# Optimization experiments

Hardware: AMD Instinct MI355X
Metric: run time of the kernel (lower is better)

## Reference

```python
import jax, jax.numpy as jnp
import numpy as np

TWO_PI = 2.0 * np.pi

def ringify(x):
    # wrap values to [-pi, pi)
    return (x + np.pi) % TWO_PI - np.pi

def complex_mean(x, axes):
    # circular mean direction: atan2(sum sin, sum ringify(cos))
    dir_x = ringify(jnp.cos(x)).sum(axis=axes)
    dir_y = jnp.sin(x).sum(axis=axes)
    return jnp.arctan2(dir_y, dir_x)

def setup_inputs() -> dict:
    key = jax.random.key(0)
    k1, k2, k3, k4 = jax.random.split(key, 4)
    B = 4096
    return {
        "x": jax.random.normal(k1, (B, 1, 28, 28), dtype=jnp.float32),
        "conv1_w": jax.random.normal(k2, (4, 1, 2, 2), dtype=jnp.float32),
        "conv2_w": jax.random.normal(k3, (8, 4, 4, 4), dtype=jnp.float32),
        "ff_w": jax.random.normal(k4, (288, 10), dtype=jnp.float32),
    }

def reference(x, conv1_w, conv2_w, ff_w):
    B = x.shape[0]
    x = ringify(x).reshape(B, 1, 28, 28)

    # --- ring conv1: 2x2 kernel, stride 2 (non-overlapping patches) ---
    # [B,1,28,28] -> [B,14,14,1,2,2]  (matches unfold(2,2,2).unfold(3,2,2).permute)
    p1 = x.reshape(B, 1, 14, 2, 14, 2).transpose(0, 2, 4, 1, 3, 5)
    w1 = conv1_w.transpose(1, 2, 3, 0)            # [1,2,2,4]
    d1 = ringify(p1[..., None] - w1)              # [B,14,14,1,2,2,4]
    h1 = complex_mean(d1, (3, 4, 5))              # [B,14,14,4]

    # --- ring conv2: 4x4 kernel, stride 2 (overlapping patches) ---
    h1 = h1.transpose(0, 3, 1, 2)                 # [B,4,14,14]
    idx = (jnp.arange(6) * 2)[:, None] + jnp.arange(4)[None, :]  # [6,4] window rows/cols
    p2 = h1[:, :, idx, :][:, :, :, :, idx]        # [B,4,6,4,6,4]
    p2 = p2.transpose(0, 2, 4, 1, 3, 5)           # [B,6,6,4,4,4]
    w2 = conv2_w.transpose(1, 2, 3, 0)            # [4,4,4,8]
    d2 = ringify(p2[..., None] - w2)              # [B,6,6,4,4,4,8]
    h2 = complex_mean(d2, (3, 4, 5))              # [B,6,6,8]

    # --- ring feed-forward ---
    f = h2.reshape(B, 288)
    d3 = ringify(f[:, :, None] - ff_w)            # [B,288,10]
    out = complex_mean(d3, (1,))                  # [B,10]
    return jnp.sin(out)
```

## Files before the change

kernel.cpp:

```cpp
#include <hip/hip_runtime.h>
#include <math.h>

#define FFT_OFF 0
#define W2_OFF 2880
#define W1_OFF 3400

__global__ void precompute_trig(const float* __restrict__ w1,
                                const float* __restrict__ w2,
                                const float* __restrict__ ff,
                                float2* __restrict__ ws) {
    int idx = blockIdx.x * blockDim.x + threadIdx.x;
    if (idx < 2880) {
        int k = idx / 10, n = idx % 10;
        float s, c; sincosf(ff[idx], &s, &c);
        ws[FFT_OFF + n * 288 + k] = make_float2(c, s);
    } else if (idx < 3392) {
        int i = idx - 2880;
        int oc = i >> 6, e = i & 63;
        float s, c; sincosf(w2[i], &s, &c);
        ws[W2_OFF + (oc >> 1) * 130 + e * 2 + (oc & 1)] = make_float2(c, s);
    } else if (idx < 3408) {
        int i = idx - 3392;
        float s, c; sincosf(w1[i], &s, &c);
        ws[W1_OFF + i] = make_float2(c, s);
    }
}

__global__ __launch_bounds__(320) void ringnn_kernel(
    const float* __restrict__ x,
    const float2* __restrict__ ws,
    float* __restrict__ out)
{
    __shared__ __align__(16) float2 trig2[520];
    __shared__ __align__(16) float2 sc1[1008];
    __shared__ __align__(16) float2 sc2[288];
    const int tid = threadIdx.x;
    const float2* __restrict__ fft = ws + FFT_OFF;
    const float2* __restrict__ w1t = ws + W1_OFF;

    int pi = (tid % 196) / 14, pj = tid % 14;
    float2 r0 = make_float2(0.f, 0.f), r1 = make_float2(0.f, 0.f);
    if (tid < 196) {
        const float* xb = x + (size_t)blockIdx.x * 784;
        r0 = *(const float2*)(xb + (2 * pi) * 28 + 2 * pj);
        r1 = *(const float2*)(xb + (2 * pi + 1) * 28 + 2 * pj);
    }

    if (tid < 260) ((float4*)trig2)[tid] = ((const float4*)(ws + W2_OFF))[tid];

    if (tid < 196) {
        float sx[4], cx[4];
        __sincosf(r0.x, &sx[0], &cx[0]);
        __sincosf(r0.y, &sx[1], &cx[1]);
        __sincosf(r1.x, &sx[2], &cx[2]);
        __sincosf(r1.y, &sx[3], &cx[3]);
        #pragma unroll
        for (int oc = 0; oc < 4; oc++) {
            float4 wa = *(const float4*)(w1t + oc * 4);
            float4 wb = *(const float4*)(w1t + oc * 4 + 2);
            float Y = 0.f, X = 0.f;
            Y = fmaf(sx[0], wa.x, fmaf(-cx[0], wa.y, Y));
            X = fmaf(cx[0], wa.x, fmaf( sx[0], wa.y, X));
            Y = fmaf(sx[1], wa.z, fmaf(-cx[1], wa.w, Y));
            X = fmaf(cx[1], wa.z, fmaf( sx[1], wa.w, X));
            Y = fmaf(sx[2], wb.x, fmaf(-cx[2], wb.y, Y));
            X = fmaf(cx[2], wb.x, fmaf( sx[2], wb.y, X));
            Y = fmaf(sx[3], wb.z, fmaf(-cx[3], wb.w, Y));
            X = fmaf(cx[3], wb.z, fmaf( sx[3], wb.w, X));
            float inv = rsqrtf(fmaxf(fmaf(X, X, Y * Y), 1e-30f));
            sc1[oc * 252 + pi * 18 + pj] = make_float2(Y * inv, X * inv);
        }
    }
    __syncthreads();

    if (tid < 96) {
        int r = tid;
        int oi = r >> 4, ojg = (r >> 3) & 1, ocp = (r >> 1) & 3, hf = r & 1;
        const float2* wbp = trig2 + ocp * 130;
        float aY[3][2] = {{0.f,0.f},{0.f,0.f},{0.f,0.f}};
        float aX[3][2] = {{0.f,0.f},{0.f,0.f},{0.f,0.f}};
        #pragma unroll
        for (int ch = 0; ch < 4; ch++) {
            #pragma unroll
            for (int kk = 0; kk < 2; kk++) {
                int ki = hf * 2 + kk;
                int base = ch * 252 + (oi * 2 + ki) * 18 + ojg * 6;
                float4 f0 = *(const float4*)(sc1 + base);
                float4 f1 = *(const float4*)(sc1 + base + 2);
                float4 f2 = *(const float4*)(sc1 + base + 4);
                float4 f3 = *(const float4*)(sc1 + base + 6);
                float ss[8] = {f0.x,f0.z,f1.x,f1.z,f2.x,f2.z,f3.x,f3.z};
                float cc[8] = {f0.y,f0.w,f1.y,f1.w,f2.y,f2.w,f3.y,f3.w};
                int e0 = ch * 16 + ki * 4;
                #pragma unroll
                for (int kj = 0; kj < 4; kj++) {
                    float4 wv = *(const float4*)(wbp + (e0 + kj) * 2);
                    #pragma unroll
                    for (int ojl = 0; ojl < 3; ojl++) {
                        float s = ss[ojl * 2 + kj], c = cc[ojl * 2 + kj];
                        aY[ojl][0] = fmaf(s, wv.x, fmaf(-c, wv.y, aY[ojl][0]));
                        aX[ojl][0] = fmaf(c, wv.x, fmaf( s, wv.y, aX[ojl][0]));
                        aY[ojl][1] = fmaf(s, wv.z, fmaf(-c, wv.w, aY[ojl][1]));
                        aX[ojl][1] = fmaf(c, wv.z, fmaf( s, wv.w, aX[ojl][1]));
                    }
                }
            }
        }
        #pragma unroll
        for (int ojl = 0; ojl < 3; ojl++) {
            float y0 = aY[ojl][0]; y0 += __shfl_xor(y0, 1);
            float y1 = aY[ojl][1]; y1 += __shfl_xor(y1, 1);
            float x0 = aX[ojl][0]; x0 += __shfl_xor(x0, 1);
            float x1 = aX[ojl][1]; x1 += __shfl_xor(x1, 1);
            float Y = hf ? y1 : y0;
            float X = hf ? x1 : x0;
            float inv = rsqrtf(fmaxf(fmaf(X, X, Y * Y), 1e-30f));
            int p = oi * 6 + ojg * 3 + ojl;
            sc2[p * 8 + ocp * 2 + hf] = make_float2(Y * inv, X * inv);
        }
    }
    __syncthreads();

    {
        int n = tid >> 5, s = tid & 31;
        const float2* wn = fft + n * 288;
        float Y = 0.f, X = 0.f;
        #pragma unroll
        for (int i = 0; i < 9; i++) {
            int k = i * 32 + s;
            float2 sc = sc2[k];
            float2 w = wn[k];
            Y = fmaf(sc.x, w.x, fmaf(-sc.y, w.y, Y));
            X = fmaf(sc.y, w.x, fmaf( sc.x, w.y, X));
        }
        #pragma unroll
        for (int off = 16; off > 0; off >>= 1) {
            Y += __shfl_down(Y, off, 32);
            X += __shfl_down(X, off, 32);
        }
        if (s == 0) {
            out[(size_t)blockIdx.x * 10 + n] =
                Y * rsqrtf(fmaxf(fmaf(X, X, Y * Y), 1e-30f));
        }
    }
}

extern "C" void kernel_launch(void* const* d_in, const int* in_sizes, int n_in,
                              void* d_out, int out_size, void* d_ws, size_t ws_size,
                              hipStream_t stream) {
    const float* x  = (const float*)d_in[0];
    const float* w1 = (const float*)d_in[1];
    const float* w2 = (const float*)d_in[2];
    const float* ff = (const float*)d_in[3];
    float* out = (float*)d_out;
    const int B = in_sizes[0] / 784;

    float2* ws = (float2*)d_ws;
    precompute_trig<<<14, 256, 0, stream>>>(w1, w2, ff, ws);
    ringnn_kernel<<<B, 320, 0, stream>>>(x, ws, out);
}
```

Measured before the change: 86.49 us.

## Shrink blocks to 128 threads and give each thread multiple work items

The block size drops from 320 to 128 threads. Each thread now handles up to two conv1 positions and up to three feed-forward reduction slots, and the weight staging becomes a strided loop. The intent is to stop wasting idle lanes in the phases that used only part of the 320 threads, and to fit more blocks per CU. In exchange the conv1 and final phases are serialized per thread, while the conv2 phase still uses only 96 threads.

```diff
diff --git a/kernel.cpp b/kernel.cpp
--- a/kernel.cpp
+++ b/kernel.cpp
@@ -26,7 +26,34 @@
     }
 }
 
-__global__ __launch_bounds__(320) void ringnn_kernel(
+__device__ __forceinline__ void conv1_pos(float2 r0, float2 r1,
+                                          const float2* __restrict__ w1t,
+                                          float2* __restrict__ sc1,
+                                          int pi, int pj) {
+    float sx[4], cx[4];
+    __sincosf(r0.x, &sx[0], &cx[0]);
+    __sincosf(r0.y, &sx[1], &cx[1]);
+    __sincosf(r1.x, &sx[2], &cx[2]);
+    __sincosf(r1.y, &sx[3], &cx[3]);
+    #pragma unroll
+    for (int oc = 0; oc < 4; oc++) {
+        float4 wa = *(const float4*)(w1t + oc * 4);
+        float4 wb = *(const float4*)(w1t + oc * 4 + 2);
+        float Y = 0.f, X = 0.f;
+        Y = fmaf(sx[0], wa.x, fmaf(-cx[0], wa.y, Y));
+        X = fmaf(cx[0], wa.x, fmaf( sx[0], wa.y, X));
+        Y = fmaf(sx[1], wa.z, fmaf(-cx[1], wa.w, Y));
+        X = fmaf(cx[1], wa.z, fmaf( sx[1], wa.w, X));
+        Y = fmaf(sx[2], wb.x, fmaf(-cx[2], wb.y, Y));
+        X = fmaf(cx[2], wb.x, fmaf( sx[2], wb.y, X));
+        Y = fmaf(sx[3], wb.z, fmaf(-cx[3], wb.w, Y));
+        X = fmaf(cx[3], wb.z, fmaf( sx[3], wb.w, X));
+        float inv = rsqrtf(fmaxf(fmaf(X, X, Y * Y), 1e-30f));
+        sc1[oc * 252 + pi * 18 + pj] = make_float2(Y * inv, X * inv);
+    }
+}
+
+__global__ __launch_bounds__(128, 4) void ringnn_kernel(
     const float* __restrict__ x,
     const float2* __restrict__ ws,
     float* __restrict__ out)
@@ -38,39 +65,24 @@
     const float2* __restrict__ fft = ws + FFT_OFF;
     const float2* __restrict__ w1t = ws + W1_OFF;
 
-    int pi = (tid % 196) / 14, pj = tid % 14;
-    float2 r0 = make_float2(0.f, 0.f), r1 = make_float2(0.f, 0.f);
-    if (tid < 196) {
-        const float* xb = x + (size_t)blockIdx.x * 784;
-        r0 = *(const float2*)(xb + (2 * pi) * 28 + 2 * pj);
-        r1 = *(const float2*)(xb + (2 * pi + 1) * 28 + 2 * pj);
+    const float* xb = x + (size_t)blockIdx.x * 784;
+    const int pi0 = tid / 14, pj0 = tid % 14;
+    float2 a0 = *(const float2*)(xb + (2 * pi0) * 28 + 2 * pj0);
+    float2 a1 = *(const float2*)(xb + (2 * pi0 + 1) * 28 + 2 * pj0);
+    const int p1 = tid + 128;
+    int pi1 = 0, pj1 = 0;
+    float2 b0 = make_float2(0.f, 0.f), b1 = make_float2(0.f, 0.f);
+    if (p1 < 196) {
+        pi1 = p1 / 14; pj1 = p1 % 14;
+        b0 = *(const float2*)(xb + (2 * pi1) * 28 + 2 * pj1);
+        b1 = *(const float2*)(xb + (2 * pi1 + 1) * 28 + 2 * pj1);
     }
 
-    if (tid < 260) ((float4*)trig2)[tid] = ((const float4*)(ws + W2_OFF))[tid];
+    for (int i = tid; i < 260; i += 128)
+        ((float4*)trig2)[i] = ((const float4*)(ws + W2_OFF))[i];
 
-    if (tid < 196) {
-        float sx[4], cx[4];
-        __sincosf(r0.x, &sx[0], &cx[0]);
-        __sincosf(r0.y, &sx[1], &cx[1]);
-        __sincosf(r1.x, &sx[2], &cx[2]);
-        __sincosf(r1.y, &sx[3], &cx[3]);
-        #pragma unroll
-        for (int oc = 0; oc < 4; oc++) {
-            float4 wa = *(const float4*)(w1t + oc * 4);
-            float4 wb = *(const float4*)(w1t + oc * 4 + 2);
-            float Y = 0.f, X = 0.f;
-            Y = fmaf(sx[0], wa.x, fmaf(-cx[0], wa.y, Y));
-            X = fmaf(cx[0], wa.x, fmaf( sx[0], wa.y, X));
-            Y = fmaf(sx[1], wa.z, fmaf(-cx[1], wa.w, Y));
-            X = fmaf(cx[1], wa.z, fmaf( sx[1], wa.w, X));
-            Y = fmaf(sx[2], wb.x, fmaf(-cx[2], wb.y, Y));
-            X = fmaf(cx[2], wb.x, fmaf( sx[2], wb.y, X));
-            Y = fmaf(sx[3], wb.z, fmaf(-cx[3], wb.w, Y));
-            X = fmaf(cx[3], wb.z, fmaf( sx[3], wb.w, X));
-            float inv = rsqrtf(fmaxf(fmaf(X, X, Y * Y), 1e-30f));
-            sc1[oc * 252 + pi * 18 + pj] = make_float2(Y * inv, X * inv);
-        }
-    }
+    conv1_pos(a0, a1, w1t, sc1, pi0, pj0);
+    if (p1 < 196) conv1_pos(b0, b1, w1t, sc1, pi1, pj1);
     __syncthreads();
 
     if (tid < 96) {
@@ -121,26 +133,30 @@
     }
     __syncthreads();
 
-    {
-        int n = tid >> 5, s = tid & 31;
-        const float2* wn = fft + n * 288;
-        float Y = 0.f, X = 0.f;
-        #pragma unroll
-        for (int i = 0; i < 9; i++) {
-            int k = i * 32 + s;
-            float2 sc = sc2[k];
-            float2 w = wn[k];
-            Y = fmaf(sc.x, w.x, fmaf(-sc.y, w.y, Y));
-            X = fmaf(sc.y, w.x, fmaf( sc.x, w.y, X));
-        }
-        #pragma unroll
-        for (int off = 16; off > 0; off >>= 1) {
-            Y += __shfl_down(Y, off, 32);
-            X += __shfl_down(X, off, 32);
-        }
-        if (s == 0) {
-            out[(size_t)blockIdx.x * 10 + n] =
-                Y * rsqrtf(fmaxf(fmaf(X, X, Y * Y), 1e-30f));
+    #pragma unroll
+    for (int rr = 0; rr < 3; rr++) {
+        int idx = tid + (rr << 7);
+        if (idx < 320) {
+            int n = idx >> 5, s = idx & 31;
+            const float2* wn = fft + n * 288;
+            float Y = 0.f, X = 0.f;
+            #pragma unroll
+            for (int i = 0; i < 9; i++) {
+                int k = i * 32 + s;
+                float2 sc = sc2[k];
+                float2 w = wn[k];
+                Y = fmaf(sc.x, w.x, fmaf(-sc.y, w.y, Y));
+                X = fmaf(sc.y, w.x, fmaf( sc.x, w.y, X));
+            }
+            #pragma unroll
+            for (int off = 16; off > 0; off >>= 1) {
+                Y += __shfl_down(Y, off, 32);
+                X += __shfl_down(X, off, 32);
+            }
+            if (s == 0) {
+                out[(size_t)blockIdx.x * 10 + n] =
+                    Y * rsqrtf(fmaxf(fmaf(X, X, Y * Y), 1e-30f));
+            }
         }
     }
 }
@@ -157,5 +173,5 @@
 
     float2* ws = (float2*)d_ws;
     precompute_trig<<<14, 256, 0, stream>>>(w1, w2, ff, ws);
-    ringnn_kernel<<<B, 320, 0, stream>>>(x, ws, out);
+    ringnn_kernel<<<B, 128, 0, stream>>>(x, ws, out);
 }
```

After: 85.01 us. No clear change (-1.7%).

## Process one image per wavefront, three per block, dropping block barriers

Applied to the files above, without the earlier changes.

Each 64-lane wavefront now handles one whole image, looping over conv1 positions, conv2 tasks and FF outputs, and each block holds three images with per-wave shared scratch. The __syncthreads between stages are replaced by a wave-local lgkmcnt wait, which removes block-wide barriers and the idle lanes left by the 320-thread layout. The cost is more serial work per wave, a larger shared-memory footprint per block, and reliance on the wave executing in lockstep for correct ordering through LDS.

```diff
diff --git a/kernel.cpp b/kernel.cpp
--- a/kernel.cpp
+++ b/kernel.cpp
@@ -26,103 +26,132 @@
     }
 }
 
-__global__ __launch_bounds__(320) void ringnn_kernel(
+__device__ __forceinline__ void conv1_pos(float2 r0, float2 r1,
+                                          const float2* __restrict__ w1t,
+                                          float2* __restrict__ sc1,
+                                          int pi, int pj) {
+    float sx[4], cx[4];
+    __sincosf(r0.x, &sx[0], &cx[0]);
+    __sincosf(r0.y, &sx[1], &cx[1]);
+    __sincosf(r1.x, &sx[2], &cx[2]);
+    __sincosf(r1.y, &sx[3], &cx[3]);
+    #pragma unroll
+    for (int oc = 0; oc < 4; oc++) {
+        float4 wa = *(const float4*)(w1t + oc * 4);
+        float4 wb = *(const float4*)(w1t + oc * 4 + 2);
+        float Y = 0.f, X = 0.f;
+        Y = fmaf(sx[0], wa.x, fmaf(-cx[0], wa.y, Y));
+        X = fmaf(cx[0], wa.x, fmaf( sx[0], wa.y, X));
+        Y = fmaf(sx[1], wa.z, fmaf(-cx[1], wa.w, Y));
+        X = fmaf(cx[1], wa.z, fmaf( sx[1], wa.w, X));
+        Y = fmaf(sx[2], wb.x, fmaf(-cx[2], wb.y, Y));
+        X = fmaf(cx[2], wb.x, fmaf( sx[2], wb.y, X));
+        Y = fmaf(sx[3], wb.z, fmaf(-cx[3], wb.w, Y));
+        X = fmaf(cx[3], wb.z, fmaf( sx[3], wb.w, X));
+        float inv = rsqrtf(fmaxf(fmaf(X, X, Y * Y), 1e-30f));
+        sc1[oc * 252 + pi * 18 + pj] = make_float2(Y * inv, X * inv);
+    }
+}
+
+__global__ __launch_bounds__(192, 4) void ringnn_kernel(
     const float* __restrict__ x,
     const float2* __restrict__ ws,
-    float* __restrict__ out)
+    float* __restrict__ out,
+    int nImg)
 {
     __shared__ __align__(16) float2 trig2[520];
-    __shared__ __align__(16) float2 sc1[1008];
-    __shared__ __align__(16) float2 sc2[288];
+    __shared__ __align__(16) float2 sc1s[3 * 1008];
+    __shared__ __align__(16) float2 sc2s[3 * 288];
     const int tid = threadIdx.x;
+    const int wave = tid >> 6, lane = tid & 63;
+    const int img = blockIdx.x * 3 + wave;
     const float2* __restrict__ fft = ws + FFT_OFF;
     const float2* __restrict__ w1t = ws + W1_OFF;
+    const bool live = (img < nImg);
 
-    int pi = (tid % 196) / 14, pj = tid % 14;
-    float2 r0 = make_float2(0.f, 0.f), r1 = make_float2(0.f, 0.f);
-    if (tid < 196) {
-        const float* xb = x + (size_t)blockIdx.x * 784;
-        r0 = *(const float2*)(xb + (2 * pi) * 28 + 2 * pj);
-        r1 = *(const float2*)(xb + (2 * pi + 1) * 28 + 2 * pj);
+    const float* xp = x + (size_t)img * 784;
+    float2 xa[4], xb[4];
+    #pragma unroll
+    for (int r = 0; r < 4; r++) {
+        int pos = lane + (r << 6);
+        xa[r] = make_float2(0.f, 0.f); xb[r] = make_float2(0.f, 0.f);
+        if (live && pos < 196) {
+            int pi = pos / 14, pj = pos % 14;
+            xa[r] = *(const float2*)(xp + (2 * pi) * 28 + 2 * pj);
+            xb[r] = *(const float2*)(xp + (2 * pi + 1) * 28 + 2 * pj);
+        }
     }
 
-    if (tid < 260) ((float4*)trig2)[tid] = ((const float4*)(ws + W2_OFF))[tid];
+    for (int i = tid; i < 260; i += 192)
+        ((float4*)trig2)[i] = ((const float4*)(ws + W2_OFF))[i];
+    __syncthreads();
+    if (!live) return;
 
-    if (tid < 196) {
-        float sx[4], cx[4];
-        __sincosf(r0.x, &sx[0], &cx[0]);
-        __sincosf(r0.y, &sx[1], &cx[1]);
-        __sincosf(r1.x, &sx[2], &cx[2]);
-        __sincosf(r1.y, &sx[3], &cx[3]);
-        #pragma unroll
-        for (int oc = 0; oc < 4; oc++) {
-            float4 wa = *(const float4*)(w1t + oc * 4);
-            float4 wb = *(const float4*)(w1t + oc * 4 + 2);
-            float Y = 0.f, X = 0.f;
-            Y = fmaf(sx[0], wa.x, fmaf(-cx[0], wa.y, Y));
-            X = fmaf(cx[0], wa.x, fmaf( sx[0], wa.y, X));
-            Y = fmaf(sx[1], wa.z, fmaf(-cx[1], wa.w, Y));
-            X = fmaf(cx[1], wa.z, fmaf( sx[1], wa.w, X));
-            Y = fmaf(sx[2], wb.x, fmaf(-cx[2], wb.y, Y));
-            X = fmaf(cx[2], wb.x, fmaf( sx[2], wb.y, X));
-            Y = fmaf(sx[3], wb.z, fmaf(-cx[3], wb.w, Y));
-            X = fmaf(cx[3], wb.z, fmaf( sx[3], wb.w, X));
-            float inv = rsqrtf(fmaxf(fmaf(X, X, Y * Y), 1e-30f));
-            sc1[oc * 252 + pi * 18 + pj] = make_float2(Y * inv, X * inv);
-        }
+    float2* __restrict__ sc1 = sc1s + wave * 1008;
+    float2* __restrict__ sc2 = sc2s + wave * 288;
+
+    #pragma unroll
+    for (int r = 0; r < 4; r++) {
+        int pos = lane + (r << 6);
+        if (pos < 196) conv1_pos(xa[r], xb[r], w1t, sc1, pos / 14, pos % 14);
     }
-    __syncthreads();
+    asm volatile("s_waitcnt lgkmcnt(0)" ::: "memory");
 
-    if (tid < 96) {
-        int r = tid;
-        int oi = r >> 4, ojg = (r >> 3) & 1, ocp = (r >> 1) & 3, hf = r & 1;
-        const float2* wbp = trig2 + ocp * 130;
-        float aY[3][2] = {{0.f,0.f},{0.f,0.f},{0.f,0.f}};
-        float aX[3][2] = {{0.f,0.f},{0.f,0.f},{0.f,0.f}};
-        #pragma unroll
-        for (int ch = 0; ch < 4; ch++) {
+    #pragma unroll
+    for (int rr = 0; rr < 2; rr++) {
+        int task = lane + (rr << 6);
+        if (task < 96) {
+            int oi = task >> 4, ojg = (task >> 3) & 1, ocp = (task >> 1) & 3, hf = task & 1;
+            const float2* wbp = trig2 + ocp * 130;
+            float aY[3][2] = {{0.f,0.f},{0.f,0.f},{0.f,0.f}};
+            float aX[3][2] = {{0.f,0.f},{0.f,0.f},{0.f,0.f}};
             #pragma unroll
-            for (int kk = 0; kk < 2; kk++) {
-                int ki = hf * 2 + kk;
-                int base = ch * 252 + (oi * 2 + ki) * 18 + ojg * 6;
-                float4 f0 = *(const float4*)(sc1 + base);
-                float4 f1 = *(const float4*)(sc1 + base + 2);
-                float4 f2 = *(const float4*)(sc1 + base + 4);
-                float4 f3 = *(const float4*)(sc1 + base + 6);
-                float ss[8] = {f0.x,f0.z,f1.x,f1.z,f2.x,f2.z,f3.x,f3.z};
-                float cc[8] = {f0.y,f0.w,f1.y,f1.w,f2.y,f2.w,f3.y,f3.w};
-                int e0 = ch * 16 + ki * 4;
+            for (int ch = 0; ch < 4; ch++) {
                 #pragma unroll
-                for (int kj = 0; kj < 4; kj++) {
-                    float4 wv = *(const float4*)(wbp + (e0 + kj) * 2);
+                for (int kk = 0; kk < 2; kk++) {
+                    int ki = hf * 2 + kk;
+                    int base = ch * 252 + (oi * 2 + ki) * 18 + ojg * 6;
+                    float4 f0 = *(const float4*)(sc1 + base);
+                    float4 f1 = *(const float4*)(sc1 + base + 2);
+                    float4 f2 = *(const float4*)(sc1 + base + 4);
+                    float4 f3 = *(const float4*)(sc1 + base + 6);
+                    float ss[8] = {f0.x,f0.z,f1.x,f1.z,f2.x,f2.z,f3.x,f3.z};
+                    float cc[8] = {f0.y,f0.w,f1.y,f1.w,f2.y,f2.w,f3.y,f3.w};
+                    int e0 = ch * 16 + ki * 4;
                     #pragma unroll
-                    for (int ojl = 0; ojl < 3; ojl++) {
-                        float s = ss[ojl * 2 + kj], c = cc[ojl * 2 + kj];
-                        aY[ojl][0] = fmaf(s, wv.x, fmaf(-c, wv.y, aY[ojl][0]));
-                        aX[ojl][0] = fmaf(c, wv.x, fmaf( s, wv.y, aX[ojl][0]));
-                        aY[ojl][1] = fmaf(s, wv.z, fmaf(-c, wv.w, aY[ojl][1]));
-                        aX[ojl][1] = fmaf(c, wv.z, fmaf( s, wv.w, aX[ojl][1]));
+                    for (int kj = 0; kj < 4; kj++) {
+                        float4 wv = *(const float4*)(wbp + (e0 + kj) * 2);
+                        #pragma unroll
+                        for (int ojl = 0; ojl < 3; ojl++) {
+                            float s = ss[ojl * 2 + kj], c = cc[ojl * 2 + kj];
+                            aY[ojl][0] = fmaf(s, wv.x, fmaf(-c, wv.y, aY[ojl][0]));
+                            aX[ojl][0] = fmaf(c, wv.x, fmaf( s, wv.y, aX[ojl][0]));
+                            aY[ojl][1] = fmaf(s, wv.z, fmaf(-c, wv.w, aY[ojl][1]));
+                            aX[ojl][1] = fmaf(c, wv.z, fmaf( s, wv.w, aX[ojl][1]));
+                        }
                     }
                 }
             }
-        }
-        #pragma unroll
-        for (int ojl = 0; ojl < 3; ojl++) {
-            float y0 = aY[ojl][0]; y0 += __shfl_xor(y0, 1);
-            float y1 = aY[ojl][1]; y1 += __shfl_xor(y1, 1);
-            float x0 = aX[ojl][0]; x0 += __shfl_xor(x0, 1);
-            float x1 = aX[ojl][1]; x1 += __shfl_xor(x1, 1);
-            float Y = hf ? y1 : y0;
-            float X = hf ? x1 : x0;
-            float inv = rsqrtf(fmaxf(fmaf(X, X, Y * Y), 1e-30f));
-            int p = oi * 6 + ojg * 3 + ojl;
-            sc2[p * 8 + ocp * 2 + hf] = make_float2(Y * inv, X * inv);
+            #pragma unroll
+            for (int ojl = 0; ojl < 3; ojl++) {
+                float y0 = aY[ojl][0]; y0 += __shfl_xor(y0, 1);
+                float y1 = aY[ojl][1]; y1 += __shfl_xor(y1, 1);
+                float x0 = aX[ojl][0]; x0 += __shfl_xor(x0, 1);
+                float x1 = aX[ojl][1]; x1 += __shfl_xor(x1, 1);
+                float Y = hf ? y1 : y0;
+                float X = hf ? x1 : x0;
+                float inv = rsqrtf(fmaxf(fmaf(X, X, Y * Y), 1e-30f));
+                int p = oi * 6 + ojg * 3 + ojl;
+                sc2[p * 8 + ocp * 2 + hf] = make_float2(Y * inv, X * inv);
+            }
         }
     }
-    __syncthreads();
+    asm volatile("s_waitcnt lgkmcnt(0)" ::: "memory");
 
-    {
-        int n = tid >> 5, s = tid & 31;
+    #pragma unroll
+    for (int rr = 0; rr < 5; rr++) {
+        int task = lane + (rr << 6);
+        int n = task >> 5, s = task & 31;
         const float2* wn = fft + n * 288;
         float Y = 0.f, X = 0.f;
         #pragma unroll
@@ -139,7 +168,7 @@
             X += __shfl_down(X, off, 32);
         }
         if (s == 0) {
-            out[(size_t)blockIdx.x * 10 + n] =
+            out[(size_t)img * 10 + n] =
                 Y * rsqrtf(fmaxf(fmaf(X, X, Y * Y), 1e-30f));
         }
     }
@@ -157,5 +186,5 @@
 
     float2* ws = (float2*)d_ws;
     precompute_trig<<<14, 256, 0, stream>>>(w1, w2, ff, ws);
-    ringnn_kernel<<<B, 320, 0, stream>>>(x, ws, out);
+    ringnn_kernel<<<(B + 2) / 3, 192, 0, stream>>>(x, ws, out, B);
 }
```

New measurement: 86.16 us. No clear change (-0.4%).

## Process eight images per block with warp-per-image stages and DPP reductions

Applied to the files above, without the earlier changes.

Restructures the ring-NN kernel so each 256-thread block handles eight images instead of one. Conv1 runs one 32-lane group per image, conv2 assigns a wave per output-channel pair with weights read from global memory instead of staged in LDS, and the feed-forward stage uses a DPP-based 32-lane reduction per image. The aim is to raise thread utilisation (the old layout left many threads idle per stage) and amortise launch and sync overhead across images. In exchange it uses much more LDS per block and caps occupancy via launch bounds. It also assumes the batch size is divisible by 8.

```diff
diff --git a/kernel.cpp b/kernel.cpp
--- a/kernel.cpp
+++ b/kernel.cpp
@@ -4,6 +4,8 @@
 #define FFT_OFF 0
 #define W2_OFF 2880
 #define W1_OFF 3400
+#define S1 786
+#define S2 292
 
 __global__ void precompute_trig(const float* __restrict__ w1,
                                 const float* __restrict__ w2,
@@ -26,121 +28,152 @@
     }
 }
 
-__global__ __launch_bounds__(320) void ringnn_kernel(
+__device__ __forceinline__ void conv1_pos(float2 r0, float2 r1,
+                                          const float2* __restrict__ w1t,
+                                          float2* __restrict__ sc1,
+                                          int pi, int pj) {
+    float sx[4], cx[4];
+    __sincosf(r0.x, &sx[0], &cx[0]);
+    __sincosf(r0.y, &sx[1], &cx[1]);
+    __sincosf(r1.x, &sx[2], &cx[2]);
+    __sincosf(r1.y, &sx[3], &cx[3]);
+    #pragma unroll
+    for (int oc = 0; oc < 4; oc++) {
+        float4 wa = *(const float4*)(w1t + oc * 4);
+        float4 wb = *(const float4*)(w1t + oc * 4 + 2);
+        float Y = 0.f, X = 0.f;
+        Y = fmaf(sx[0], wa.x, fmaf(-cx[0], wa.y, Y));
+        X = fmaf(cx[0], wa.x, fmaf( sx[0], wa.y, X));
+        Y = fmaf(sx[1], wa.z, fmaf(-cx[1], wa.w, Y));
+        X = fmaf(cx[1], wa.z, fmaf( sx[1], wa.w, X));
+        Y = fmaf(sx[2], wb.x, fmaf(-cx[2], wb.y, Y));
+        X = fmaf(cx[2], wb.x, fmaf( sx[2], wb.y, X));
+        Y = fmaf(sx[3], wb.z, fmaf(-cx[3], wb.w, Y));
+        X = fmaf(cx[3], wb.z, fmaf( sx[3], wb.w, X));
+        float inv = rsqrtf(fmaxf(fmaf(X, X, Y * Y), 1e-30f));
+        sc1[oc * 196 + pi * 14 + pj] = make_float2(Y * inv, X * inv);
+    }
+}
+
+template <int CTRL>
+__device__ __forceinline__ float dpp_add(float v) {
+    return v + __int_as_float(__builtin_amdgcn_mov_dpp(
+                   __float_as_int(v), CTRL, 0xF, 0xF, true));
+}
+__device__ __forceinline__ float reduce32(float v) {
+    v = dpp_add<0x111>(v);
+    v = dpp_add<0x112>(v);
+    v = dpp_add<0x114>(v);
+    v = dpp_add<0x118>(v);
+    v = dpp_add<0x142>(v);
+    return v;
+}
+
+__global__ __launch_bounds__(256, 2) void ringnn_kernel(
     const float* __restrict__ x,
     const float2* __restrict__ ws,
     float* __restrict__ out)
 {
-    __shared__ __align__(16) float2 trig2[520];
-    __shared__ __align__(16) float2 sc1[1008];
-    __shared__ __align__(16) float2 sc2[288];
+    __shared__ __align__(16) float2 sc1[8 * S1];
+    __shared__ __align__(16) float2 sc2[8 * S2];
     const int tid = threadIdx.x;
+    const int g = tid >> 5, s = tid & 31;
+    const size_t imgBase = (size_t)blockIdx.x * 8;
     const float2* __restrict__ fft = ws + FFT_OFF;
     const float2* __restrict__ w1t = ws + W1_OFF;
 
-    int pi = (tid % 196) / 14, pj = tid % 14;
-    float2 r0 = make_float2(0.f, 0.f), r1 = make_float2(0.f, 0.f);
-    if (tid < 196) {
-        const float* xb = x + (size_t)blockIdx.x * 784;
-        r0 = *(const float2*)(xb + (2 * pi) * 28 + 2 * pj);
-        r1 = *(const float2*)(xb + (2 * pi + 1) * 28 + 2 * pj);
-    }
-
-    if (tid < 260) ((float4*)trig2)[tid] = ((const float4*)(ws + W2_OFF))[tid];
-
-    if (tid < 196) {
-        float sx[4], cx[4];
-        __sincosf(r0.x, &sx[0], &cx[0]);
-        __sincosf(r0.y, &sx[1], &cx[1]);
-        __sincosf(r1.x, &sx[2], &cx[2]);
-        __sincosf(r1.y, &sx[3], &cx[3]);
+    {
+        const float* xp = x + (imgBase + g) * 784;
+        float2* s1 = sc1 + g * S1;
         #pragma unroll
-        for (int oc = 0; oc < 4; oc++) {
-            float4 wa = *(const float4*)(w1t + oc * 4);
-            float4 wb = *(const float4*)(w1t + oc * 4 + 2);
-            float Y = 0.f, X = 0.f;
-            Y = fmaf(sx[0], wa.x, fmaf(-cx[0], wa.y, Y));
-            X = fmaf(cx[0], wa.x, fmaf( sx[0], wa.y, X));
-            Y = fmaf(sx[1], wa.z, fmaf(-cx[1], wa.w, Y));
-            X = fmaf(cx[1], wa.z, fmaf( sx[1], wa.w, X));
-            Y = fmaf(sx[2], wb.x, fmaf(-cx[2], wb.y, Y));
-            X = fmaf(cx[2], wb.x, fmaf( sx[2], wb.y, X));
-            Y = fmaf(sx[3], wb.z, fmaf(-cx[3], wb.w, Y));
-            X = fmaf(cx[3], wb.z, fmaf( sx[3], wb.w, X));
-            float inv = rsqrtf(fmaxf(fmaf(X, X, Y * Y), 1e-30f));
-            sc1[oc * 252 + pi * 18 + pj] = make_float2(Y * inv, X * inv);
-        }
-    }
-    __syncthreads();
-
-    if (tid < 96) {
-        int r = tid;
-        int oi = r >> 4, ojg = (r >> 3) & 1, ocp = (r >> 1) & 3, hf = r & 1;
-        const float2* wbp = trig2 + ocp * 130;
-        float aY[3][2] = {{0.f,0.f},{0.f,0.f},{0.f,0.f}};
-        float aX[3][2] = {{0.f,0.f},{0.f,0.f},{0.f,0.f}};
-        #pragma unroll
-        for (int ch = 0; ch < 4; ch++) {
-            #pragma unroll
-            for (int kk = 0; kk < 2; kk++) {
-                int ki = hf * 2 + kk;
-                int base = ch * 252 + (oi * 2 + ki) * 18 + ojg * 6;
-                float4 f0 = *(const float4*)(sc1 + base);
-                float4 f1 = *(const float4*)(sc1 + base + 2);
-                float4 f2 = *(const float4*)(sc1 + base + 4);
-                float4 f3 = *(const float4*)(sc1 + base + 6);
-                float ss[8] = {f0.x,f0.z,f1.x,f1.z,f2.x,f2.z,f3.x,f3.z};
-                float cc[8] = {f0.y,f0.w,f1.y,f1.w,f2.y,f2.w,f3.y,f3.w};
-                int e0 = ch * 16 + ki * 4;
-                #pragma unroll
-                for (int kj = 0; kj < 4; kj++) {
-                    float4 wv = *(const float4*)(wbp + (e0 + kj) * 2);
-                    #pragma unroll
-                    for (int ojl = 0; ojl < 3; ojl++) {
-                        float s = ss[ojl * 2 + kj], c = cc[ojl * 2 + kj];
-                        aY[ojl][0] = fmaf(s, wv.x, fmaf(-c, wv.y, aY[ojl][0]));
-                        aX[ojl][0] = fmaf(c, wv.x, fmaf( s, wv.y, aX[ojl][0]));
-                        aY[ojl][1] = fmaf(s, wv.z, fmaf(-c, wv.w, aY[ojl][1]));
-                        aX[ojl][1] = fmaf(c, wv.z, fmaf( s, wv.w, aX[ojl][1]));
-                    }
-                }
+        for (int r = 0; r < 7; r++) {
+            int pos = r * 32 + s;
+            if (pos < 196) {
+                int pi = pos / 14, pj = pos % 14;
+                float2 r0 = *(const float2*)(xp + (2 * pi) * 28 + 2 * pj);
+                float2 r1 = *(const float2*)(xp + (2 * pi + 1) * 28 + 2 * pj);
+                conv1_pos(r0, r1, w1t, s1, pi, pj);
             }
-        }
-        #pragma unroll
-        for (int ojl = 0; ojl < 3; ojl++) {
-            float y0 = aY[ojl][0]; y0 += __shfl_xor(y0, 1);
-            float y1 = aY[ojl][1]; y1 += __shfl_xor(y1, 1);
-            float x0 = aX[ojl][0]; x0 += __shfl_xor(x0, 1);
-            float x1 = aX[ojl][1]; x1 += __shfl_xor(x1, 1);
-            float Y = hf ? y1 : y0;
-            float X = hf ? x1 : x0;
-            float inv = rsqrtf(fmaxf(fmaf(X, X, Y * Y), 1e-30f));
-            int p = oi * 6 + ojg * 3 + ojl;
-            sc2[p * 8 + ocp * 2 + hf] = make_float2(Y * inv, X * inv);
         }
     }
     __syncthreads();
 
     {
-        int n = tid >> 5, s = tid & 31;
-        const float2* wn = fft + n * 288;
-        float Y = 0.f, X = 0.f;
+        const int ocp = __builtin_amdgcn_readfirstlane(tid >> 6);
+        const int l = tid & 63;
+        const int imq = l >> 4;
+        const int oi  = (l >> 1) & 7;
+        const int ojg = l & 1;
+        const float2* __restrict__ wbp = ws + W2_OFF + ocp * 130;
         #pragma unroll
-        for (int i = 0; i < 9; i++) {
-            int k = i * 32 + s;
-            float2 sc = sc2[k];
-            float2 w = wn[k];
-            Y = fmaf(sc.x, w.x, fmaf(-sc.y, w.y, Y));
-            X = fmaf(sc.y, w.x, fmaf( sc.x, w.y, X));
+        for (int rr = 0; rr < 2; rr++) {
+            const int im = rr * 4 + imq;
+            if (oi < 6) {
+                const float2* __restrict__ s1p = sc1 + im * S1;
+                float aY[3][2] = {{0.f,0.f},{0.f,0.f},{0.f,0.f}};
+                float aX[3][2] = {{0.f,0.f},{0.f,0.f},{0.f,0.f}};
+                #pragma unroll
+                for (int ch = 0; ch < 4; ch++) {
+                    #pragma unroll
+                    for (int ki = 0; ki < 4; ki++) {
+                        int base = ch * 196 + (oi * 2 + ki) * 14 + ojg * 6;
+                        float4 f0 = *(const float4*)(s1p + base);
+                        float4 f1 = *(const float4*)(s1p + base + 2);
+                        float4 f2 = *(const float4*)(s1p + base + 4);
+                        float4 f3 = *(const float4*)(s1p + base + 6);
+                        float ss[8] = {f0.x,f0.z,f1.x,f1.z,f2.x,f2.z,f3.x,f3.z};
+                        float cc[8] = {f0.y,f0.w,f1.y,f1.w,f2.y,f2.w,f3.y,f3.w};
+                        int e0 = ch * 16 + ki * 4;
+                        #pragma unroll
+                        for (int kj = 0; kj < 4; kj++) {
+                            float4 wv = *(const float4*)(wbp + (e0 + kj) * 2);
+                            #pragma unroll
+                            for (int ojl = 0; ojl < 3; ojl++) {
+                                float sv = ss[ojl * 2 + kj], cv = cc[ojl * 2 + kj];
+                                aY[ojl][0] = fmaf(sv, wv.x, fmaf(-cv, wv.y, aY[ojl][0]));
+                                aX[ojl][0] = fmaf(cv, wv.x, fmaf( sv, wv.y, aX[ojl][0]));
+                                aY[ojl][1] = fmaf(sv, wv.z, fmaf(-cv, wv.w, aY[ojl][1]));
+                                aX[ojl][1] = fmaf(cv, wv.z, fmaf( sv, wv.w, aX[ojl][1]));
+                            }
+                        }
+                    }
+                }
+                float2* s2p = sc2 + im * S2;
+                #pragma unroll
+                for (int ojl = 0; ojl < 3; ojl++) {
+                    float Y0 = aY[ojl][0], X0 = aX[ojl][0];
+                    float Y1 = aY[ojl][1], X1 = aX[ojl][1];
+                    float i0 = rsqrtf(fmaxf(fmaf(X0, X0, Y0 * Y0), 1e-30f));
+                    float i1 = rsqrtf(fmaxf(fmaf(X1, X1, Y1 * Y1), 1e-30f));
+                    int p = oi * 6 + ojg * 3 + ojl;
+                    *(float4*)(s2p + p * 8 + ocp * 2) =
+                        make_float4(Y0 * i0, X0 * i0, Y1 * i1, X1 * i1);
+                }
+            }
         }
+    }
+    __syncthreads();
+
+    {
+        const float2* __restrict__ s2p = sc2 + g * S2;
+        const size_t obase = (imgBase + g) * 10;
         #pragma unroll
-        for (int off = 16; off > 0; off >>= 1) {
-            Y += __shfl_down(Y, off, 32);
-            X += __shfl_down(X, off, 32);
-        }
-        if (s == 0) {
-            out[(size_t)blockIdx.x * 10 + n] =
-                Y * rsqrtf(fmaxf(fmaf(X, X, Y * Y), 1e-30f));
+        for (int n = 0; n < 10; n++) {
+            const float2* __restrict__ wn = fft + n * 288;
+            float Y = 0.f, X = 0.f;
+            #pragma unroll
+            for (int i = 0; i < 9; i++) {
+                int k = i * 32 + s;
+                float2 sc = s2p[k];
+                float2 w = wn[k];
+                Y = fmaf(sc.x, w.x, fmaf(-sc.y, w.y, Y));
+                X = fmaf(sc.y, w.x, fmaf( sc.x, w.y, X));
+            }
+            Y = reduce32(Y);
+            X = reduce32(X);
+            if (s == 31) {
+                out[obase + n] = Y * rsqrtf(fmaxf(fmaf(X, X, Y * Y), 1e-30f));
+            }
         }
     }
 }
@@ -157,5 +190,5 @@
 
     float2* ws = (float2*)d_ws;
     precompute_trig<<<14, 256, 0, stream>>>(w1, w2, ff, ws);
-    ringnn_kernel<<<B, 320, 0, stream>>>(x, ws, out);
+    ringnn_kernel<<<B / 8, 256, 0, stream>>>(x, ws, out);
 }
```

Measured after the change: 90.30 us. 1.04x slower.
